# Kernel tuning notes

Hardware: AMD Instinct MI355X
Metric: run time of the kernel (lower is better)

## Reference

```python
import jax, jax.numpy as jnp
import numpy as np

# dims: B batch, T seq, DM d_model, H kv heads, D head dim
B, T, DM = 4, 2048, 768
H, D = 4, 64          # n_kv_heads, d_head = d_model // n_heads = 768 // 12
DIM = H * D           # 256


def setup_inputs() -> dict:
    key = jax.random.key(0)
    kx, kq, kk, kv, ko, kg = jax.random.split(key, 6)
    s = 0.02  # init scale for weights
    return {
        "x": jax.random.normal(kx, (B, T, DM), jnp.float32),
        "Wq": jax.random.normal(kq, (DM, DIM), jnp.float32) * s,
        "Wk": jax.random.normal(kk, (DM, DIM), jnp.float32) * s,
        "Wv": jax.random.normal(kv, (DM, DIM), jnp.float32) * s,
        "Wo": jax.random.normal(ko, (DIM, DM), jnp.float32) * s,
        "Wg": jax.random.normal(kg, (DM, DM), jnp.float32) * s,
    }


def _feature_map(x):
    # F.elu(x) + 1.0  (strictly positive features)
    return jax.nn.elu(x) + 1.0


def reference(x, Wq, Wk, Wv, Wo, Wg):
    Bx, Tx, _ = x.shape
    q = _feature_map((x @ Wq).reshape(Bx, Tx, H, D))
    k = _feature_map((x @ Wk).reshape(Bx, Tx, H, D))
    v = (x @ Wv).reshape(Bx, Tx, H, D)

    # time-major for scan: [T, B, H, D]
    qT = q.transpose(1, 0, 2, 3)
    kT = k.transpose(1, 0, 2, 3)
    vT = v.transpose(1, 0, 2, 3)

    S0 = jnp.zeros((Bx, H, D, D), x.dtype)  # running sum of k v^T
    z0 = jnp.zeros((Bx, H, D), x.dtype)     # running sum of k

    def step(carry, inp):
        S, z = carry
        qi, ki, vi = inp  # each [B, H, D]
        S = S + ki[..., :, None] * vi[..., None, :]   # outer product update
        z = z + ki
        num = jnp.einsum('bhd,bhde->bhe', qi, S)
        den = jnp.maximum(jnp.sum(qi * z, axis=-1), 1e-6)  # clamp(min=1e-6)
        return (S, z), num / den[..., None]

    (_, _), outT = jax.lax.scan(step, (S0, z0), (qT, kT, vT))

    out = outT.transpose(1, 0, 2, 3).reshape(Bx, Tx, DIM)  # [B, T, H*D]
    gate = jax.nn.sigmoid(x @ Wg)
    return (out @ Wo) * gate
```

## Files before the change

### kernel.cpp

```cpp
#include <hip/hip_runtime.h>
#include <math.h>

typedef __attribute__((ext_vector_type(8))) short bf16x8;
typedef __attribute__((ext_vector_type(4))) float f32x4;

namespace {
constexpr int Bb  = 4;
constexpr int Tt  = 2048;
constexpr int DM  = 768;
constexpr int Hh  = 4;
constexpr int Dd  = 64;
constexpr int DIM = 256;
constexpr int BT  = Bb * Tt;
constexpr int CH  = 64;
constexpr int NC  = Tt / CH;
constexpr int NQKVG = 1536;
constexpr int MT  = BT / 128;
}

__device__ __forceinline__ float elu1(float x) { return x > 0.f ? x + 1.f : expf(x); }

__device__ __forceinline__ unsigned short f2bf(float f) {
  unsigned int x = __float_as_uint(f);
  unsigned int r = (x + 0x7fffu + ((x >> 16) & 1u)) >> 16;
  return (unsigned short)r;
}
__device__ __forceinline__ float bf2f(unsigned short u) {
  return __uint_as_float((unsigned int)u << 16);
}

__device__ __forceinline__ void gload16(const void* g, void* l) {
  __builtin_amdgcn_global_load_lds(
      (const __attribute__((address_space(1))) void*)g,
      (__attribute__((address_space(3))) void*)l, 16, 0, 0);
}

__device__ __forceinline__ void stage2(const short* __restrict__ Ag, size_t lda,
                                       const short* __restrict__ Bg, size_t ldb,
                                       int k0, short* as, short* bs, int w, int l) {
  const int c16 = (l & 7) ^ (l >> 3);
#pragma unroll
  for (int i = 0; i < 4; ++i) {
    int seg = w * 4 + i;
    int row = seg * 8 + (l >> 3);
    gload16(Ag + (size_t)row * lda + k0 + c16 * 8, (char*)as + seg * 1024);
    gload16(Bg + (size_t)row * ldb + k0 + c16 * 8, (char*)bs + seg * 1024);
  }
}

__device__ __forceinline__ void mma64(const short* as, const short* bs,
                                      f32x4 (&acc)[4][4],
                                      int wr, int wc, int lr, int lg) {
  const int sa = lr & 7;
#pragma unroll
  for (int ks = 0; ks < 2; ++ks) {
    bf16x8 af[4], bf[4];
#pragma unroll
    for (int mi = 0; mi < 4; ++mi)
      af[mi] = *(const bf16x8*)&as[(wr * 64 + mi * 16 + lr) * 64 +
                                   ((ks * 4 + lg) ^ sa) * 8];
#pragma unroll
    for (int ni = 0; ni < 4; ++ni)
      bf[ni] = *(const bf16x8*)&bs[(wc * 64 + ni * 16 + lr) * 64 +
                                   ((ks * 4 + lg) ^ sa) * 8];
#pragma unroll
    for (int mi = 0; mi < 4; ++mi)
#pragma unroll
      for (int ni = 0; ni < 4; ++ni)
        acc[mi][ni] = __builtin_amdgcn_mfma_f32_16x16x32_bf16(
            af[mi], bf[ni], acc[mi][ni], 0, 0, 0);
  }
}

__device__ __forceinline__ void xcd_tile(int bid, int& mt, int& nt) {
  int xcd = bid & 7;
  int idx = bid >> 3;
  mt = xcd * 8 + (idx & 7);
  nt = idx >> 3;
}

template <int NT>
__device__ __forceinline__ void kloop(const short* Ag, size_t lda,
                                      const short* Bg, size_t ldb,
                                      short* As0, short* As1, short* Bs0,
                                      short* Bs1, f32x4 (&acc)[4][4], int w,
                                      int l, int wr, int wc, int lr, int lg) {
  stage2(Ag, lda, Bg, ldb, 0, As0, Bs0, w, l);
  stage2(Ag, lda, Bg, ldb, 64, As1, Bs1, w, l);
#pragma unroll
  for (int t = 0; t < NT; ++t) {
    short* as = (t & 1) ? As1 : As0;
    short* bs = (t & 1) ? Bs1 : Bs0;
    if (t + 1 < NT)
      asm volatile("s_waitcnt vmcnt(8)" ::: "memory");
    else
      asm volatile("s_waitcnt vmcnt(0)" ::: "memory");
    __builtin_amdgcn_s_barrier();
    __builtin_amdgcn_sched_barrier(0);
    mma64(as, bs, acc, wr, wc, lr, lg);
    __builtin_amdgcn_sched_barrier(0);
    __builtin_amdgcn_s_barrier();
    if (t + 2 < NT) stage2(Ag, lda, Bg, ldb, (t + 2) * 64, as, bs, w, l);
  }
}

__global__ __launch_bounds__(256) void k_cast(const float* __restrict__ in,
                                              unsigned short* __restrict__ out,
                                              int n8) {
  int i = blockIdx.x * 256 + threadIdx.x;
  if (i >= n8) return;
  const float4* p = (const float4*)(in + (size_t)i * 8);
  float4 a = p[0], b = p[1];
  union { unsigned short u[8]; uint4 v; } r;
  r.u[0] = f2bf(a.x); r.u[1] = f2bf(a.y); r.u[2] = f2bf(a.z); r.u[3] = f2bf(a.w);
  r.u[4] = f2bf(b.x); r.u[5] = f2bf(b.y); r.u[6] = f2bf(b.z); r.u[7] = f2bf(b.w);
  *(uint4*)(out + (size_t)i * 8) = r.v;
}

__global__ __launch_bounds__(256) void k_convAll(
    const float* __restrict__ Wq, const float* __restrict__ Wk,
    const float* __restrict__ Wv, const float* __restrict__ Wg,
    const float* __restrict__ Wo, unsigned short* __restrict__ WT,
    unsigned short* __restrict__ WoT) {
  __shared__ float t[32][33];
  int idx = blockIdx.x;
  const float* src;
  unsigned short* out;
  int K, N, n_off, ldo;
  if (idx < 576) {
    int z = idx / 192;
    idx %= 192;
    src = (z == 0) ? Wq : (z == 1) ? Wk : Wv;
    out = WT; K = 768; N = 256; n_off = z * 256; ldo = 768;
  } else if (idx < 1152) {
    idx -= 576;
    src = Wg; out = WT; K = 768; N = 768; n_off = 768; ldo = 768;
  } else {
    idx -= 1152;
    src = Wo; out = WoT; K = 256; N = 768; n_off = 0; ldo = 256;
  }
  int kt = idx % (K / 32), nt = idx / (K / 32);
  int k0 = kt * 32, n0 = nt * 32;
  const int tx = threadIdx.x, ty = threadIdx.y;
  for (int i = ty; i < 32; i += 8)
    t[i][tx] = src[(size_t)(k0 + i) * N + n0 + tx];
  __syncthreads();
  for (int i = ty; i < 32; i += 8)
    out[(size_t)(n_off + n0 + i) * ldo + k0 + tx] = f2bf(t[tx][i]);
}

__global__ __launch_bounds__(256) void k_gemm1(
    const unsigned short* __restrict__ xb, const unsigned short* __restrict__ WT,
    unsigned short* __restrict__ Q, unsigned short* __restrict__ K,
    unsigned short* __restrict__ V, unsigned short* __restrict__ G) {
  __shared__ __align__(16) char smem[65536];
  short* As0 = (short*)smem;
  short* As1 = (short*)(smem + 16384);
  short* Bs0 = (short*)(smem + 32768);
  short* Bs1 = (short*)(smem + 49152);
  const int tid = threadIdx.x;
  const int w = tid >> 6, l = tid & 63;
  const int lr = l & 15, lg = l >> 4;
  const int wr = w >> 1, wc = w & 1;
  int mt, nt;
  xcd_tile(blockIdx.x, mt, nt);
  const int m0 = mt * 128, n0 = nt * 128;
  const short* Ag = (const short*)xb + (size_t)m0 * DM;
  const short* Bg = (const short*)WT + (size_t)n0 * DM;

  f32x4 acc[4][4];
#pragma unroll
  for (int i = 0; i < 4; ++i)
#pragma unroll
    for (int j = 0; j < 4; ++j) acc[i][j] = (f32x4){0.f, 0.f, 0.f, 0.f};

  kloop<DM / 64>(Ag, DM, Bg, DM, As0, As1, Bs0, Bs1, acc, w, l, wr, wc, lr, lg);
  __syncthreads();

  const int ttype = (n0 < 512) ? 0 : (n0 < 768) ? 1 : 2;
  unsigned short* Cs = (unsigned short*)smem;
#pragma unroll
  for (int mi = 0; mi < 4; ++mi)
#pragma unroll
    for (int ni = 0; ni < 4; ++ni)
#pragma unroll
      for (int r = 0; r < 4; ++r) {
        float v = acc[mi][ni][r];
        if (ttype == 0) v = elu1(v);
        else if (ttype == 2) v = 1.f / (1.f + expf(-v));
        Cs[(wr * 64 + mi * 16 + lg * 4 + r) * 128 + wc * 64 + ni * 16 + lr] =
            f2bf(v);
      }
  __syncthreads();
  unsigned short* dst;
  int ldd, cb;
  if (n0 < 256)      { dst = Q; ldd = DIM; cb = n0; }
  else if (n0 < 512) { dst = K; ldd = DIM; cb = n0 - 256; }
  else if (n0 < 768) { dst = V; ldd = DIM; cb = n0 - 512; }
  else               { dst = G; ldd = DM;  cb = n0 - 768; }
  const uint4* Cv = (const uint4*)Cs;
#pragma unroll
  for (int i = 0; i < 8; ++i) {
    int idx = tid + i * 256;
    int urow = idx >> 4, uc = idx & 15;
    *(uint4*)(dst + (size_t)(m0 + urow) * ldd + cb + uc * 8) = Cv[idx];
  }
}

__global__ __launch_bounds__(256) void k_chunksum(
    const unsigned short* __restrict__ K, const unsigned short* __restrict__ V,
    float* __restrict__ Sc, float* __restrict__ zc) {
  __shared__ float Ks[CH][68];
  __shared__ float Vs[CH][68];
  const int c = blockIdx.x, h = blockIdx.y, b = blockIdx.z;
  const int tx = threadIdx.x, ty = threadIdx.y;
  const int tid = ty * 16 + tx;
  const int t0 = c * CH;
#pragma unroll
  for (int l = 0; l < 4; ++l) {
    int idx = tid + l * 256;
    int d4 = idx & 15, t = idx >> 4;
    size_t o = (size_t)(b * Tt + t0 + t) * DIM + h * Dd + d4 * 4;
    short4 k4 = *(const short4*)(K + o);
    short4 v4 = *(const short4*)(V + o);
    Ks[t][d4 * 4 + 0] = bf2f(k4.x); Ks[t][d4 * 4 + 1] = bf2f(k4.y);
    Ks[t][d4 * 4 + 2] = bf2f(k4.z); Ks[t][d4 * 4 + 3] = bf2f(k4.w);
    Vs[t][d4 * 4 + 0] = bf2f(v4.x); Vs[t][d4 * 4 + 1] = bf2f(v4.y);
    Vs[t][d4 * 4 + 2] = bf2f(v4.z); Vs[t][d4 * 4 + 3] = bf2f(v4.w);
  }
  __syncthreads();
  float acc[4][4] = {};
  for (int t = 0; t < CH; ++t) {
    float4 k4 = *(const float4*)&Ks[t][ty * 4];
    float4 v4 = *(const float4*)&Vs[t][tx * 4];
    float kv[4] = {k4.x, k4.y, k4.z, k4.w};
    float vv[4] = {v4.x, v4.y, v4.z, v4.w};
#pragma unroll
    for (int i = 0; i < 4; ++i)
#pragma unroll
      for (int j = 0; j < 4; ++j) acc[i][j] += kv[i] * vv[j];
  }
  const size_t base = ((size_t)(b * Hh + h) * NC + c) * (Dd * Dd);
#pragma unroll
  for (int i = 0; i < 4; ++i) {
    float4 s4 = make_float4(acc[i][0], acc[i][1], acc[i][2], acc[i][3]);
    *(float4*)&Sc[base + (size_t)(ty * 4 + i) * Dd + tx * 4] = s4;
  }
  if (tid < Dd) {
    float s = 0.f;
    for (int t = 0; t < CH; ++t) s += Ks[t][tid];
    zc[((size_t)(b * Hh + h) * NC + c) * Dd + tid] = s;
  }
}

__global__ __launch_bounds__(256) void k_scan(float* __restrict__ Sc,
                                              float* __restrict__ zc) {
  const int bh = blockIdx.x;
  const int o = blockIdx.y * 256 + threadIdx.x;
  const size_t base = (size_t)bh * NC * (Dd * Dd) + o;
  float v[NC];
#pragma unroll
  for (int c = 0; c < NC; ++c) v[c] = Sc[base + (size_t)c * (Dd * Dd)];
  float run = 0.f;
#pragma unroll
  for (int c = 0; c < NC; ++c) {
    Sc[base + (size_t)c * (Dd * Dd)] = run;
    run += v[c];
  }
  if (blockIdx.y == 0 && threadIdx.x < Dd) {
    float rz = 0.f;
    for (int c = 0; c < NC; ++c) {
      size_t oz = ((size_t)bh * NC + c) * Dd + threadIdx.x;
      float cur = zc[oz];
      zc[oz] = rz;
      rz += cur;
    }
  }
}

__global__ __launch_bounds__(256) void k_out(
    const unsigned short* __restrict__ Q, const unsigned short* __restrict__ K,
    const unsigned short* __restrict__ V, const float* __restrict__ Sc,
    const float* __restrict__ zc, unsigned short* __restrict__ O) {
  __shared__ float Qs[CH][68];
  __shared__ float KVs[CH * 68];
  __shared__ float As[CH][68];
  __shared__ float Ss[Dd][68];
  __shared__ float zs[Dd];
  __shared__ float dens[CH];
  const int c = blockIdx.x, h = blockIdx.y, b = blockIdx.z;
  const int tx = threadIdx.x, ty = threadIdx.y;
  const int tid = ty * 16 + tx;
  const int t0 = c * CH;

#pragma unroll
  for (int l = 0; l < 4; ++l) {
    int idx = tid + l * 256;
    int d4 = idx & 15, t = idx >> 4;
    size_t o = (size_t)(b * Tt + t0 + t) * DIM + h * Dd + d4 * 4;
    short4 q4 = *(const short4*)(Q + o);
    short4 k4 = *(const short4*)(K + o);
    Qs[t][d4 * 4 + 0] = bf2f(q4.x); Qs[t][d4 * 4 + 1] = bf2f(q4.y);
    Qs[t][d4 * 4 + 2] = bf2f(q4.z); Qs[t][d4 * 4 + 3] = bf2f(q4.w);
    KVs[(d4 * 4 + 0) * 65 + t] = bf2f(k4.x);
    KVs[(d4 * 4 + 1) * 65 + t] = bf2f(k4.y);
    KVs[(d4 * 4 + 2) * 65 + t] = bf2f(k4.z);
    KVs[(d4 * 4 + 3) * 65 + t] = bf2f(k4.w);
  }
  __syncthreads();

  float acc[4][4] = {};
  for (int d0 = 0; d0 < Dd; d0 += 4) {
    float4 q4[4];
#pragma unroll
    for (int i = 0; i < 4; ++i) q4[i] = *(const float4*)&Qs[ty * 4 + i][d0];
#pragma unroll
    for (int dd = 0; dd < 4; ++dd) {
      int d = d0 + dd;
      float kv[4];
#pragma unroll
      for (int j = 0; j < 4; ++j) kv[j] = KVs[d * 65 + tx * 4 + j];
#pragma unroll
      for (int i = 0; i < 4; ++i) {
        float qv = ((const float*)&q4[i])[dd];
#pragma unroll
        for (int j = 0; j < 4; ++j) acc[i][j] += qv * kv[j];
      }
    }
  }
#pragma unroll
  for (int i = 0; i < 4; ++i)
#pragma unroll
    for (int j = 0; j < 4; ++j) {
      int ti = ty * 4 + i, sj = tx * 4 + j;
      As[ti][sj] = (sj <= ti) ? acc[i][j] : 0.f;
    }
  __syncthreads();

#pragma unroll
  for (int l = 0; l < 4; ++l) {
    int idx = tid + l * 256;
    int d4 = idx & 15, t = idx >> 4;
    size_t o = (size_t)(b * Tt + t0 + t) * DIM + h * Dd + d4 * 4;
    short4 v4 = *(const short4*)(V + o);
    KVs[t * 68 + d4 * 4 + 0] = bf2f(v4.x);
    KVs[t * 68 + d4 * 4 + 1] = bf2f(v4.y);
    KVs[t * 68 + d4 * 4 + 2] = bf2f(v4.z);
    KVs[t * 68 + d4 * 4 + 3] = bf2f(v4.w);
  }
  const size_t sbase = ((size_t)(b * Hh + h) * NC + c) * (Dd * Dd);
#pragma unroll
  for (int l = 0; l < 4; ++l) {
    int idx = tid + l * 256;
    int e4 = idx & 15, dd = idx >> 4;
    float4 s4 = *(const float4*)&Sc[sbase + (size_t)dd * Dd + e4 * 4];
    Ss[dd][e4 * 4 + 0] = s4.x; Ss[dd][e4 * 4 + 1] = s4.y;
    Ss[dd][e4 * 4 + 2] = s4.z; Ss[dd][e4 * 4 + 3] = s4.w;
  }
  if (tid < Dd) zs[tid] = zc[((size_t)(b * Hh + h) * NC + c) * Dd + tid];
  __syncthreads();

  if (tid < CH) {
    int i = tid;
    float rs = 0.f;
    for (int j = 0; j < CH; ++j) rs += As[i][j];
    float qz = 0.f;
    for (int d = 0; d < Dd; ++d) qz += Qs[i][d] * zs[d];
    dens[i] = fmaxf(rs + qz, 1e-6f);
  }
  float oacc[4][4] = {};
  for (int j = 0; j < CH; ++j) {
    float4 v4 = *(const float4*)&KVs[j * 68 + tx * 4];
    float vv[4] = {v4.x, v4.y, v4.z, v4.w};
    float av[4];
#pragma unroll
    for (int i = 0; i < 4; ++i) av[i] = As[ty * 4 + i][j];
#pragma unroll
    for (int i = 0; i < 4; ++i)
#pragma unroll
      for (int jj = 0; jj < 4; ++jj) oacc[i][jj] += av[i] * vv[jj];
  }
  for (int d = 0; d < Dd; ++d) {
    float4 s4 = *(const float4*)&Ss[d][tx * 4];
    float sv[4] = {s4.x, s4.y, s4.z, s4.w};
    float qv[4];
#pragma unroll
    for (int i = 0; i < 4; ++i) qv[i] = Qs[ty * 4 + i][d];
#pragma unroll
    for (int i = 0; i < 4; ++i)
#pragma unroll
      for (int jj = 0; jj < 4; ++jj) oacc[i][jj] += qv[i] * sv[jj];
  }
  __syncthreads();
#pragma unroll
  for (int i = 0; i < 4; ++i) {
    float inv = 1.f / dens[ty * 4 + i];
#pragma unroll
    for (int jj = 0; jj < 4; ++jj) {
      O[(size_t)(b * Tt + t0 + ty * 4 + i) * DIM + h * Dd + tx * 4 + jj] =
          f2bf(oacc[i][jj] * inv);
    }
  }
}

__global__ __launch_bounds__(256) void k_gemm2(
    const unsigned short* __restrict__ Ob, const unsigned short* __restrict__ WoT,
    const unsigned short* __restrict__ G, float* __restrict__ out) {
  __shared__ __align__(16) char smem[65536];
  short* As0 = (short*)smem;
  short* As1 = (short*)(smem + 16384);
  short* Bs0 = (short*)(smem + 32768);
  short* Bs1 = (short*)(smem + 49152);
  const int tid = threadIdx.x;
  const int w = tid >> 6, l = tid & 63;
  const int lr = l & 15, lg = l >> 4;
  const int wr = w >> 1, wc = w & 1;
  int mt, nt;
  xcd_tile(blockIdx.x, mt, nt);
  const int m0 = mt * 128, n0 = nt * 128;
  const short* Ag = (const short*)Ob + (size_t)m0 * DIM;
  const short* Bg = (const short*)WoT + (size_t)n0 * DIM;

  f32x4 acc[4][4];
#pragma unroll
  for (int i = 0; i < 4; ++i)
#pragma unroll
    for (int j = 0; j < 4; ++j) acc[i][j] = (f32x4){0.f, 0.f, 0.f, 0.f};

  kloop<DIM / 64>(Ag, DIM, Bg, DIM, As0, As1, Bs0, Bs1, acc, w, l, wr, wc, lr, lg);
  __syncthreads();

  float* Cf = (float*)smem;
#pragma unroll
  for (int mi = 0; mi < 4; ++mi)
#pragma unroll
    for (int ni = 0; ni < 4; ++ni)
#pragma unroll
      for (int r = 0; r < 4; ++r)
        Cf[(wr * 64 + mi * 16 + lg * 4 + r) * 128 + wc * 64 + ni * 16 + lr] =
            acc[mi][ni][r];
  __syncthreads();
  const float4* Cv = (const float4*)Cf;
#pragma unroll
  for (int i = 0; i < 16; ++i) {
    int idx = tid + i * 256;
    int urow = idx >> 5, uc = idx & 31;
    float4 cv = Cv[idx];
    size_t go = (size_t)(m0 + urow) * DM + n0 + uc * 4;
    short4 g4 = *(const short4*)(G + go);
    float4 ov;
    ov.x = cv.x * bf2f(g4.x);
    ov.y = cv.y * bf2f(g4.y);
    ov.z = cv.z * bf2f(g4.z);
    ov.w = cv.w * bf2f(g4.w);
    *(float4*)(out + go) = ov;
  }
}

extern "C" void kernel_launch(void* const* d_in, const int* in_sizes, int n_in,
                              void* d_out, int out_size, void* d_ws,
                              size_t ws_size, hipStream_t stream) {
  const float* x  = (const float*)d_in[0];
  const float* Wq = (const float*)d_in[1];
  const float* Wk = (const float*)d_in[2];
  const float* Wv = (const float*)d_in[3];
  const float* Wo = (const float*)d_in[4];
  const float* Wg = (const float*)d_in[5];
  float* out = (float*)d_out;

  char* p = (char*)d_ws;
  size_t off = 0;
  auto alloc = [&](size_t bytes) {
    void* r = p + off;
    off = (off + bytes + 255) & ~(size_t)255;
    return r;
  };
  unsigned short* xb  = (unsigned short*)alloc((size_t)BT * DM * 2);
  unsigned short* WT  = (unsigned short*)alloc((size_t)NQKVG * DM * 2);
  unsigned short* WoT = (unsigned short*)alloc((size_t)DM * DIM * 2);
  unsigned short* Q   = (unsigned short*)alloc((size_t)BT * DIM * 2);
  unsigned short* Kf  = (unsigned short*)alloc((size_t)BT * DIM * 2);
  unsigned short* Vf  = (unsigned short*)alloc((size_t)BT * DIM * 2);
  unsigned short* G   = (unsigned short*)alloc((size_t)BT * DM * 2);
  unsigned short* Ob  = (unsigned short*)alloc((size_t)BT * DIM * 2);
  float* Sc = (float*)alloc((size_t)Bb * Hh * NC * Dd * Dd * 4);
  float* zc = (float*)alloc((size_t)Bb * Hh * NC * Dd * 4);

  k_cast<<<dim3((BT * DM / 8 + 255) / 256), dim3(256), 0, stream>>>(x, xb, BT * DM / 8);
  k_convAll<<<dim3(1344), dim3(32, 8), 0, stream>>>(Wq, Wk, Wv, Wg, Wo, WT, WoT);

  k_gemm1<<<dim3(MT * (NQKVG / 128)), dim3(256), 0, stream>>>(
      xb, WT, Q, Kf, Vf, G);

  dim3 blk(16, 16);
  k_chunksum<<<dim3(NC, Hh, Bb), blk, 0, stream>>>(Kf, Vf, Sc, zc);
  k_scan<<<dim3(Bb * Hh, Dd * Dd / 256), dim3(256), 0, stream>>>(Sc, zc);
  k_out<<<dim3(NC, Hh, Bb), blk, 0, stream>>>(Q, Kf, Vf, Sc, zc, Ob);

  k_gemm2<<<dim3(MT * (DM / 128)), dim3(256), 0, stream>>>(Ob, WoT, G, out);
}
```

Baseline: 90.36 us.

## Restructure GEMM k-loop to issue next loads before MFMA and merge prep kernels

The GEMM main loop now reads all LDS fragments into registers first, waits for them, and then issues the next global-to-LDS prefetch before running the MFMAs, with raised wave priority during the MFMA block. Load addresses are precomputed once in a Stage struct. The separate cast and weight-transpose kernels are merged into one launch. This aims to overlap global loads with matrix math and cut launch and address overhead, at the cost of more live registers for the doubled fragment arrays.

```diff
diff --git a/kernel.cpp b/kernel.cpp
--- a/kernel.cpp
+++ b/kernel.cpp
@@ -35,42 +35,29 @@
       (__attribute__((address_space(3))) void*)l, 16, 0, 0);
 }
 
-__device__ __forceinline__ void stage2(const short* __restrict__ Ag, size_t lda,
-                                       const short* __restrict__ Bg, size_t ldb,
-                                       int k0, short* as, short* bs, int w, int l) {
-  const int c16 = (l & 7) ^ (l >> 3);
-#pragma unroll
-  for (int i = 0; i < 4; ++i) {
-    int seg = w * 4 + i;
-    int row = seg * 8 + (l >> 3);
-    gload16(Ag + (size_t)row * lda + k0 + c16 * 8, (char*)as + seg * 1024);
-    gload16(Bg + (size_t)row * ldb + k0 + c16 * 8, (char*)bs + seg * 1024);
-  }
-}
-
-__device__ __forceinline__ void mma64(const short* as, const short* bs,
-                                      f32x4 (&acc)[4][4],
-                                      int wr, int wc, int lr, int lg) {
-  const int sa = lr & 7;
-#pragma unroll
-  for (int ks = 0; ks < 2; ++ks) {
-    bf16x8 af[4], bf[4];
-#pragma unroll
-    for (int mi = 0; mi < 4; ++mi)
-      af[mi] = *(const bf16x8*)&as[(wr * 64 + mi * 16 + lr) * 64 +
-                                   ((ks * 4 + lg) ^ sa) * 8];
-#pragma unroll
-    for (int ni = 0; ni < 4; ++ni)
-      bf[ni] = *(const bf16x8*)&bs[(wc * 64 + ni * 16 + lr) * 64 +
-                                   ((ks * 4 + lg) ^ sa) * 8];
-#pragma unroll
-    for (int mi = 0; mi < 4; ++mi)
-#pragma unroll
-      for (int ni = 0; ni < 4; ++ni)
-        acc[mi][ni] = __builtin_amdgcn_mfma_f32_16x16x32_bf16(
-            af[mi], bf[ni], acc[mi][ni], 0, 0, 0);
-  }
-}
+struct Stage {
+  const short* a[4];
+  const short* b[4];
+  int seg;
+  __device__ __forceinline__ void init(const short* Ag, size_t lda,
+                                       const short* Bg, size_t ldb, int w, int l) {
+    const int c16 = (l & 7) ^ (l >> 3);
+    seg = w * 4;
+#pragma unroll
+    for (int i = 0; i < 4; ++i) {
+      int row = (seg + i) * 8 + (l >> 3);
+      a[i] = Ag + (size_t)row * lda + c16 * 8;
+      b[i] = Bg + (size_t)row * ldb + c16 * 8;
+    }
+  }
+  __device__ __forceinline__ void issue(int k0, short* as, short* bs) const {
+#pragma unroll
+    for (int i = 0; i < 4; ++i) {
+      gload16(a[i] + k0, (char*)as + (seg + i) * 1024);
+      gload16(b[i] + k0, (char*)bs + (seg + i) * 1024);
+    }
+  }
+};
 
 __device__ __forceinline__ void xcd_tile(int bid, int& mt, int& nt) {
   int xcd = bid & 7;
@@ -80,13 +67,13 @@
 }
 
 template <int NT>
-__device__ __forceinline__ void kloop(const short* Ag, size_t lda,
-                                      const short* Bg, size_t ldb,
-                                      short* As0, short* As1, short* Bs0,
-                                      short* Bs1, f32x4 (&acc)[4][4], int w,
-                                      int l, int wr, int wc, int lr, int lg) {
-  stage2(Ag, lda, Bg, ldb, 0, As0, Bs0, w, l);
-  stage2(Ag, lda, Bg, ldb, 64, As1, Bs1, w, l);
+__device__ __forceinline__ void kloop(const Stage& st, short* As0, short* As1,
+                                      short* Bs0, short* Bs1,
+                                      f32x4 (&acc)[4][4], int wr, int wc,
+                                      int lr, int lg) {
+  const int sa = lr & 7;
+  st.issue(0, As0, Bs0);
+  st.issue(64, As1, Bs1);
 #pragma unroll
   for (int t = 0; t < NT; ++t) {
     short* as = (t & 1) ? As1 : As0;
@@ -96,34 +83,54 @@
     else
       asm volatile("s_waitcnt vmcnt(0)" ::: "memory");
     __builtin_amdgcn_s_barrier();
-    __builtin_amdgcn_sched_barrier(0);
-    mma64(as, bs, acc, wr, wc, lr, lg);
+    bf16x8 af[2][4], bf[2][4];
+#pragma unroll
+    for (int ks = 0; ks < 2; ++ks) {
+#pragma unroll
+      for (int mi = 0; mi < 4; ++mi)
+        af[ks][mi] = *(const bf16x8*)&as[(wr * 64 + mi * 16 + lr) * 64 +
+                                         ((ks * 4 + lg) ^ sa) * 8];
+#pragma unroll
+      for (int ni = 0; ni < 4; ++ni)
+        bf[ks][ni] = *(const bf16x8*)&bs[(wc * 64 + ni * 16 + lr) * 64 +
+                                         ((ks * 4 + lg) ^ sa) * 8];
+    }
+    asm volatile("s_waitcnt lgkmcnt(0)" ::: "memory");
     __builtin_amdgcn_sched_barrier(0);
     __builtin_amdgcn_s_barrier();
-    if (t + 2 < NT) stage2(Ag, lda, Bg, ldb, (t + 2) * 64, as, bs, w, l);
-  }
-}
-
-__global__ __launch_bounds__(256) void k_cast(const float* __restrict__ in,
-                                              unsigned short* __restrict__ out,
-                                              int n8) {
-  int i = blockIdx.x * 256 + threadIdx.x;
-  if (i >= n8) return;
-  const float4* p = (const float4*)(in + (size_t)i * 8);
-  float4 a = p[0], b = p[1];
-  union { unsigned short u[8]; uint4 v; } r;
-  r.u[0] = f2bf(a.x); r.u[1] = f2bf(a.y); r.u[2] = f2bf(a.z); r.u[3] = f2bf(a.w);
-  r.u[4] = f2bf(b.x); r.u[5] = f2bf(b.y); r.u[6] = f2bf(b.z); r.u[7] = f2bf(b.w);
-  *(uint4*)(out + (size_t)i * 8) = r.v;
-}
-
-__global__ __launch_bounds__(256) void k_convAll(
-    const float* __restrict__ Wq, const float* __restrict__ Wk,
-    const float* __restrict__ Wv, const float* __restrict__ Wg,
-    const float* __restrict__ Wo, unsigned short* __restrict__ WT,
+    if (t + 2 < NT) st.issue((t + 2) * 64, as, bs);
+    __builtin_amdgcn_s_setprio(1);
+#pragma unroll
+    for (int ks = 0; ks < 2; ++ks)
+#pragma unroll
+      for (int mi = 0; mi < 4; ++mi)
+#pragma unroll
+        for (int ni = 0; ni < 4; ++ni)
+          acc[mi][ni] = __builtin_amdgcn_mfma_f32_16x16x32_bf16(
+              af[ks][mi], bf[ks][ni], acc[mi][ni], 0, 0, 0);
+    __builtin_amdgcn_s_setprio(0);
+  }
+}
+
+__global__ __launch_bounds__(256) void k_prep(
+    const float* __restrict__ x, const float* __restrict__ Wq,
+    const float* __restrict__ Wk, const float* __restrict__ Wv,
+    const float* __restrict__ Wg, const float* __restrict__ Wo,
+    unsigned short* __restrict__ xb, unsigned short* __restrict__ WT,
     unsigned short* __restrict__ WoT) {
+  int bid = blockIdx.x;
+  if (bid < 3072) {
+    int i = bid * 256 + threadIdx.x;
+    const float4* p = (const float4*)(x + (size_t)i * 8);
+    float4 a = p[0], b = p[1];
+    union { unsigned short u[8]; uint4 v; } r;
+    r.u[0] = f2bf(a.x); r.u[1] = f2bf(a.y); r.u[2] = f2bf(a.z); r.u[3] = f2bf(a.w);
+    r.u[4] = f2bf(b.x); r.u[5] = f2bf(b.y); r.u[6] = f2bf(b.z); r.u[7] = f2bf(b.w);
+    *(uint4*)(xb + (size_t)i * 8) = r.v;
+    return;
+  }
   __shared__ float t[32][33];
-  int idx = blockIdx.x;
+  int idx = bid - 3072;
   const float* src;
   unsigned short* out;
   int K, N, n_off, ldo;
@@ -141,7 +148,7 @@
   }
   int kt = idx % (K / 32), nt = idx / (K / 32);
   int k0 = kt * 32, n0 = nt * 32;
-  const int tx = threadIdx.x, ty = threadIdx.y;
+  const int tx = threadIdx.x & 31, ty = threadIdx.x >> 5;
   for (int i = ty; i < 32; i += 8)
     t[i][tx] = src[(size_t)(k0 + i) * N + n0 + tx];
   __syncthreads();
@@ -165,8 +172,10 @@
   int mt, nt;
   xcd_tile(blockIdx.x, mt, nt);
   const int m0 = mt * 128, n0 = nt * 128;
-  const short* Ag = (const short*)xb + (size_t)m0 * DM;
-  const short* Bg = (const short*)WT + (size_t)n0 * DM;
+
+  Stage st;
+  st.init((const short*)xb + (size_t)m0 * DM, DM,
+          (const short*)WT + (size_t)n0 * DM, DM, w, l);
 
   f32x4 acc[4][4];
 #pragma unroll
@@ -174,7 +183,7 @@
 #pragma unroll
     for (int j = 0; j < 4; ++j) acc[i][j] = (f32x4){0.f, 0.f, 0.f, 0.f};
 
-  kloop<DM / 64>(Ag, DM, Bg, DM, As0, As1, Bs0, Bs1, acc, w, l, wr, wc, lr, lg);
+  kloop<DM / 64>(st, As0, As1, Bs0, Bs1, acc, wr, wc, lr, lg);
   __syncthreads();
 
   const int ttype = (n0 < 512) ? 0 : (n0 < 768) ? 1 : 2;
@@ -418,8 +427,10 @@
   int mt, nt;
   xcd_tile(blockIdx.x, mt, nt);
   const int m0 = mt * 128, n0 = nt * 128;
-  const short* Ag = (const short*)Ob + (size_t)m0 * DIM;
-  const short* Bg = (const short*)WoT + (size_t)n0 * DIM;
+
+  Stage st;
+  st.init((const short*)Ob + (size_t)m0 * DIM, DIM,
+          (const short*)WoT + (size_t)n0 * DIM, DIM, w, l);
 
   f32x4 acc[4][4];
 #pragma unroll
@@ -427,7 +438,7 @@
 #pragma unroll
     for (int j = 0; j < 4; ++j) acc[i][j] = (f32x4){0.f, 0.f, 0.f, 0.f};
 
-  kloop<DIM / 64>(Ag, DIM, Bg, DIM, As0, As1, Bs0, Bs1, acc, w, l, wr, wc, lr, lg);
+  kloop<DIM / 64>(st, As0, As1, Bs0, Bs1, acc, wr, wc, lr, lg);
   __syncthreads();
 
   float* Cf = (float*)smem;
@@ -486,8 +497,8 @@
   float* Sc = (float*)alloc((size_t)Bb * Hh * NC * Dd * Dd * 4);
   float* zc = (float*)alloc((size_t)Bb * Hh * NC * Dd * 4);
 
-  k_cast<<<dim3((BT * DM / 8 + 255) / 256), dim3(256), 0, stream>>>(x, xb, BT * DM / 8);
-  k_convAll<<<dim3(1344), dim3(32, 8), 0, stream>>>(Wq, Wk, Wv, Wg, Wo, WT, WoT);
+  k_prep<<<dim3(3072 + 1344), dim3(256), 0, stream>>>(x, Wq, Wk, Wv, Wg, Wo,
+                                                      xb, WT, WoT);
 
   k_gemm1<<<dim3(MT * (NQKVG / 128)), dim3(256), 0, stream>>>(
       xb, WT, Q, Kf, Vf, G);
```

Measured after the change: 86.81 us. 1.04x faster.
